# Performance work log

Measured on AMD Instinct MI355X. Metric: run time of the kernel, lower is better.

Reference implementation:

```python
import jax, jax.numpy as jnp
import numpy as np

TAU = 0.07      # temperature from __init__ default
TOP_K = 10      # hardcoded k in torch.topk
DIAG_FILL = -10.0
TOP_SIM_VAL = 0.75


def setup_inputs() -> dict:
    key = jax.random.key(0)
    k1, k2 = jax.random.split(key)
    z1 = jax.random.normal(k1, (4096, 512), dtype=jnp.float32)
    z2 = jax.random.normal(k2, (4096, 512), dtype=jnp.float32)
    return {"z1": z1, "z2": z2}


def reference(z1, z2):
    # AllGather is identity on a single device; grad_scaling=False.
    z = jnp.concatenate([z1, z2], axis=0)                      # [n, d]
    # F.normalize(dim=1): divide by L2 norm (eps-clamped)
    norm = jnp.maximum(jnp.linalg.norm(z, axis=1, keepdims=True), 1e-12)
    z = z / norm
    n = z.shape[0]
    half = n // 2

    # labels: ones at offsets +n/2 and -n/2 == identity rolled by n/2
    labels = jnp.roll(jnp.eye(n, dtype=z.dtype), half, axis=1)  # [n, n]

    sim = z @ z.T                                               # [n, n]

    # top_k_based_on_cos_sim branch: softmax of raw sim (diag still present)
    cos_sim = jax.nn.softmax(sim, axis=1)
    idx = jnp.arange(n)
    # branch mask: 0 on same-half blocks, 1 on cross-half blocks
    mask = ((idx[:, None] < half) ^ (idx[None, :] < half)).astype(z.dtype)
    cos_sim = cos_sim * mask
    _, top_idx = jax.lax.top_k(cos_sim, TOP_K)                  # [n, K]
    top_sim = jnp.zeros((n, n), dtype=z.dtype).at[idx[:, None], top_idx].set(TOP_SIM_VAL)
    labels = jnp.maximum(labels, top_sim)

    # fill diagonal with -10, scale by temperature, row log-softmax
    sim = sim.at[idx, idx].set(DIAG_FILL) / TAU
    logp = jax.nn.log_softmax(sim, axis=1)
    loss = -jnp.sum(logp * labels) / n
    return loss
```

## Files before the change

### kernel.cpp

```cpp
#include <hip/hip_runtime.h>
#include <hip/hip_bf16.h>
#include <stdint.h>

#define N_TOTAL 8192
#define HALF_N  4096
#define DIM     512
#define INV_TAU (1.0f/0.07f)

typedef __attribute__((ext_vector_type(4))) int   i32x4;

#define AS1 __attribute__((address_space(1)))
#define AS3 __attribute__((address_space(3)))

__device__ __forceinline__ uint32_t umax32(uint32_t a, uint32_t b) { return a > b ? a : b; }
__device__ __forceinline__ uint32_t umin32(uint32_t a, uint32_t b) { return a < b ? a : b; }

__device__ __forceinline__ float decode_key(uint32_t key)
{
    ushort h = (key & 0x8000u) ? (ushort)(key ^ 0x8000u) : (ushort)(key ^ 0xFFFFu);
    return (float)(*(_Float16*)&h);
}

__global__ __launch_bounds__(256) void norm_kernel(const float* __restrict__ z1,
                                                   const float* __restrict__ z2,
                                                   char* __restrict__ zq,
                                                   float* __restrict__ inv_qn,
                                                   float* __restrict__ rowsum)
{
    if (threadIdx.x < 4) rowsum[blockIdx.x * 4 + threadIdx.x] = 0.f;

    int row  = blockIdx.x * 4 + (threadIdx.x >> 6);
    int lane = threadIdx.x & 63;
    const float* src = (row < HALF_N) ? (z1 + (size_t)row * DIM)
                                      : (z2 + (size_t)(row - HALF_N) * DIM);
    const float4* p = (const float4*)src;
    float4 a = p[lane * 2];
    float4 b = p[lane * 2 + 1];
    float ss = a.x*a.x + a.y*a.y + a.z*a.z + a.w*a.w
             + b.x*b.x + b.y*b.y + b.z*b.z + b.w*b.w;
#pragma unroll
    for (int o = 1; o < 64; o <<= 1) ss += __shfl_xor(ss, o);
    float sc = 127.0f / fmaxf(sqrtf(ss), 1e-12f);

    float v[8] = {a.x*sc, a.y*sc, a.z*sc, a.w*sc, b.x*sc, b.y*sc, b.z*sc, b.w*sc};
    char c8[8];
    int qq = 0;
#pragma unroll
    for (int j = 0; j < 8; j++) {
        int qi = (int)rintf(v[j]);
        qq += qi * qi;
        c8[j] = (char)qi;
    }
#pragma unroll
    for (int o = 1; o < 64; o <<= 1) qq += __shfl_xor(qq, o);
    if (lane == 0) inv_qn[row] = 1.0f / sqrtf(fmaxf((float)qq, 1.0f));

    *(uint2*)(zq + (size_t)row * DIM + lane * 8) = *(const uint2*)c8;
}

__global__ __launch_bounds__(256, 4) void gemm_kernel(const char* __restrict__ zq,
                                                      const float* __restrict__ inv_qn,
                                                      float* __restrict__ rowsum,
                                                      uint2* __restrict__ partial,
                                                      float* __restrict__ pos_sim)
{
    int orig = blockIdx.x;
    int bid  = (orig & 7) * 260 + (orig >> 3);

    int by = (int)(64.5f - sqrtf(4160.25f - 2.0f * (float)bid));
    int off = 64 * by - (by * (by - 1)) / 2;
    if (off > bid) { --by; off = 64 * by - (by * (by - 1)) / 2; }
    else {
        int offn = 64 * (by + 1) - ((by + 1) * by) / 2;
        if (offn <= bid) { ++by; off = offn; }
    }
    int bx = by + (bid - off);

    const int brow = by * 128;
    const int bcol = bx * 128;

    __shared__ char As[2][128 * 64];
    __shared__ char Bs[2][128 * 64];

    const int t    = threadIdx.x;
    const int w    = t >> 6;
    const int lane = t & 63;
    const int wr   = w >> 1, wc = w & 1;

    i32x4 acc[4][4] = {};

    const int c0 = t, c1 = 256 + t;
    const int r0 = c0 >> 2, r1 = c1 >> 2;
    const int q0 = (c0 & 3) ^ ((r0 >> 1) & 3);
    const int q1 = (c1 & 3) ^ ((r1 >> 1) & 3);
    const size_t gaA0 = (size_t)(brow + r0) * DIM + q0 * 16;
    const size_t gaA1 = (size_t)(brow + r1) * DIM + q1 * 16;
    const size_t gaB0 = (size_t)(bcol + r0) * DIM + q0 * 16;
    const size_t gaB1 = (size_t)(bcol + r1) * DIM + q1 * 16;
    const int l0 = (w * 64) * 16;
    const int l1 = (256 + w * 64) * 16;

#define STAGE(buf, ko) do {                                                        \
    __builtin_amdgcn_global_load_lds((const AS1 uint32_t*)(zq + gaA0 + (ko)),      \
        (AS3 uint32_t*)((char*)As[buf] + l0), 16, 0, 0);                           \
    __builtin_amdgcn_global_load_lds((const AS1 uint32_t*)(zq + gaA1 + (ko)),      \
        (AS3 uint32_t*)((char*)As[buf] + l1), 16, 0, 0);                           \
    __builtin_amdgcn_global_load_lds((const AS1 uint32_t*)(zq + gaB0 + (ko)),      \
        (AS3 uint32_t*)((char*)Bs[buf] + l0), 16, 0, 0);                           \
    __builtin_amdgcn_global_load_lds((const AS1 uint32_t*)(zq + gaB1 + (ko)),      \
        (AS3 uint32_t*)((char*)Bs[buf] + l1), 16, 0, 0);                           \
} while (0)

    STAGE(0, 0);
    __syncthreads();

    int cur = 0;
    for (int kt = 0; kt < DIM / 64; ++kt) {
        if (kt + 1 < DIM / 64) STAGE(cur ^ 1, (kt + 1) * 64);

        i32x4 av[4], bv[4];
#pragma unroll
        for (int m = 0; m < 4; m++) {
            int ro = wr * 64 + m * 16 + (lane & 15);
            int s  = (lane >> 4) ^ ((ro >> 1) & 3);
            av[m] = *(const i32x4*)(As[cur] + ro * 64 + s * 16);
        }
#pragma unroll
        for (int n = 0; n < 4; n++) {
            int ro = wc * 64 + n * 16 + (lane & 15);
            int s  = (lane >> 4) ^ ((ro >> 1) & 3);
            bv[n] = *(const i32x4*)(Bs[cur] + ro * 64 + s * 16);
        }
#pragma unroll
        for (int m = 0; m < 4; m++)
#pragma unroll
            for (int n = 0; n < 4; n++)
                acc[m][n] = __builtin_amdgcn_mfma_i32_16x16x64_i8(av[m], bv[n], acc[m][n], 0, 0, 0);

        __syncthreads();
        cur ^= 1;
    }
#undef STAGE

    const bool is_cross = (brow < HALF_N) && (bcol >= HALF_N);
    const bool off_diag = (bx != by);

    float invc[4];
#pragma unroll
    for (int n = 0; n < 4; n++)
        invc[n] = inv_qn[bcol + wc * 64 + n * 16 + (lane & 15)];

    float    cs[4] = {0.f, 0.f, 0.f, 0.f};
    uint32_t s1[4] = {0u, 0u, 0u, 0u};
    uint32_t s2[4] = {0u, 0u, 0u, 0u};

#pragma unroll
    for (int m = 0; m < 4; m++) {
#pragma unroll
        for (int r = 0; r < 4; r++) {
            int grow = brow + wr * 64 + m * 16 + ((lane >> 4) << 2) + r;
            float invr = inv_qn[grow];
            float rs = 0.f;
            uint32_t t1 = 0u, t2 = 0u;
#pragma unroll
            for (int n = 0; n < 4; n++) {
                int gcol = bcol + wc * 64 + n * 16 + (lane & 15);
                float v  = (float)acc[m][n][r] * (invr * invc[n]);
                float e  = (grow == gcol) ? 0.f : __expf(v * INV_TAU);
                rs += e;
                cs[n] += e;
                if (is_cross) {
                    int cidx = gcol - HALF_N;
                    ushort h;
                    *(_Float16*)&h = (_Float16)v;
                    uint32_t key = ((uint32_t)(ushort)(h ^ (ushort)((ushort)((short)h >> 15) | 0x8000))) << 16;
                    uint32_t xr = key | (uint32_t)(4095 - cidx);
                    uint32_t mn = umin32(t1, xr);
                    t1 = umax32(t1, xr);
                    t2 = umax32(t2, mn);
                    uint32_t xc = key | (uint32_t)(4095 - grow);
                    mn = umin32(s1[n], xc);
                    s1[n] = umax32(s1[n], xc);
                    s2[n] = umax32(s2[n], mn);
                    if (cidx == grow) { pos_sim[grow] = v; pos_sim[gcol] = v; }
                }
            }
            rs += __shfl_xor(rs, 1);
            rs += __shfl_xor(rs, 2);
            rs += __shfl_xor(rs, 4);
            rs += __shfl_xor(rs, 8);
            if ((lane & 15) == 0) atomicAdd(&rowsum[grow], rs);

            if (is_cross) {
#pragma unroll
                for (int o = 1; o < 16; o <<= 1) {
                    uint32_t o1 = __shfl_xor(t1, o);
                    uint32_t o2 = __shfl_xor(t2, o);
                    uint32_t nt2 = umax32(umin32(t1, o1), umax32(t2, o2));
                    t1 = umax32(t1, o1);
                    t2 = nt2;
                }
                if ((lane & 15) == 0)
                    partial[((size_t)grow << 6) + (bx - 32) * 2 + wc] = make_uint2(t1, t2);
            }
        }
    }

    if (off_diag) {
#pragma unroll
        for (int n = 0; n < 4; n++) {
            float c = cs[n];
            c += __shfl_xor(c, 16);
            c += __shfl_xor(c, 32);
            uint32_t a1 = s1[n], a2 = s2[n];
            if (is_cross) {
#pragma unroll
                for (int o = 16; o < 64; o <<= 1) {
                    uint32_t o1 = __shfl_xor(a1, o);
                    uint32_t o2 = __shfl_xor(a2, o);
                    uint32_t nt2 = umax32(umin32(a1, o1), umax32(a2, o2));
                    a1 = umax32(a1, o1);
                    a2 = nt2;
                }
            }
            if (lane < 16) {
                int gcol = bcol + wc * 64 + n * 16 + lane;
                atomicAdd(&rowsum[gcol], c);
                if (is_cross)
                    partial[((size_t)gcol << 6) + by * 2 + wr] = make_uint2(a1, a2);
            }
        }
    }
}

__global__ __launch_bounds__(256) void topk_loss_kernel(const uint2* __restrict__ partial,
                                                        const float* __restrict__ pos_sim,
                                                        const float* __restrict__ rowsum,
                                                        float* __restrict__ contrib)
{
    int i    = blockIdx.x * 4 + (threadIdx.x >> 6);
    int lane = threadIdx.x & 63;

    uint2 p = partial[((size_t)i << 6) + lane];
    uint32_t t1 = p.x, t2 = p.y;

    int posidx = i & (HALF_N - 1);
    float S10 = 0.f; int posflag = 0;
#pragma unroll
    for (int tc = 0; tc < 10; tc++) {
        uint32_t b = umax32(t1, t2);
#pragma unroll
        for (int o = 32; o; o >>= 1)
            b = umax32(b, __shfl_xor(b, o));
        bool w1 = (b == t1);
        bool w2 = (b == t2);
        t1 = w1 ? t2 : t1;
        t2 = (w1 | w2) ? 0u : t2;

        int idx = 4095 - (int)(b & 0xFFFFu);
        S10 += decode_key(b >> 16);
        posflag |= (idx == posidx) ? 1 : 0;
    }

    if (lane == 0) {
        float ps  = pos_sim[i];
        float lse = logf(rowsum[i]);
        float L   = 1.0f + 0.75f * (10 - posflag);
        float sll = INV_TAU * (ps + 0.75f * (S10 - posflag * ps));
        contrib[i] = L * lse - sll;
    }
}

__global__ __launch_bounds__(256) void reduce_kernel(const float* __restrict__ contrib,
                                                     float* __restrict__ out)
{
    int t = threadIdx.x;
    float s = 0.f;
    for (int j = t; j < N_TOTAL; j += 256) s += contrib[j];
#pragma unroll
    for (int o = 1; o < 64; o <<= 1) s += __shfl_xor(s, o);
    __shared__ float wsum[4];
    if ((t & 63) == 0) wsum[t >> 6] = s;
    __syncthreads();
    if (t == 0) out[0] = (wsum[0] + wsum[1] + wsum[2] + wsum[3]) * (1.0f / N_TOTAL);
}

extern "C" void kernel_launch(void* const* d_in, const int* in_sizes, int n_in,
                              void* d_out, int out_size, void* d_ws, size_t ws_size,
                              hipStream_t stream)
{
    const float* z1 = (const float*)d_in[0];
    const float* z2 = (const float*)d_in[1];
    float* out = (float*)d_out;

    char* ws = (char*)d_ws;
    char*   zq      = ws;
    float*  rowsum  = (float*)(ws + 4194304);
    float*  pos_sim = (float*)(ws + 4227072);
    float*  inv_qn  = (float*)(ws + 4259840);
    uint2*  partial = (uint2*)(ws + 4292608);
    float*  contrib = (float*)(ws + 8486912);

    norm_kernel<<<N_TOTAL / 4, 256, 0, stream>>>(z1, z2, zq, inv_qn, rowsum);
    gemm_kernel<<<2080, 256, 0, stream>>>(zq, inv_qn, rowsum, partial, pos_sim);
    topk_loss_kernel<<<N_TOTAL / 4, 256, 0, stream>>>(partial, pos_sim, rowsum, contrib);
    reduce_kernel<<<1, 256, 0, stream>>>(contrib, out);
}
```

Measured before the change: 92.04 us.

## Fold temperature into exp2 scale, raise GEMM occupancy, fuse reduce into top-k kernel

The norm kernel now stores the per-row inverse norm premultiplied by log2(e)/tau, so the GEMM epilogue can call exp2 directly and skip a multiply. The raw similarity is recovered by a constant multiply only on cross blocks. Launch bounds go from 4 to 5 waves, and the column accumulators are split into two sets to shorten dependency chains. The separate reduce kernel is removed: each top-k block handles 32 rows and atomically adds its share into the output, which the norm kernel zeroes. The changes add register pressure at higher occupancy and make the final sum order nondeterministic.

```diff
diff --git a/kernel.cpp b/kernel.cpp
--- a/kernel.cpp
+++ b/kernel.cpp
@@ -6,6 +6,8 @@
 #define HALF_N  4096
 #define DIM     512
 #define INV_TAU (1.0f/0.07f)
+#define EXP2_SCALE  4.5398160046388386f
+#define SIM_FROM_VE 0.0485203026391962f
 
 typedef __attribute__((ext_vector_type(4))) int   i32x4;
 
@@ -24,10 +26,12 @@
 __global__ __launch_bounds__(256) void norm_kernel(const float* __restrict__ z1,
                                                    const float* __restrict__ z2,
                                                    char* __restrict__ zq,
-                                                   float* __restrict__ inv_qn,
-                                                   float* __restrict__ rowsum)
+                                                   float* __restrict__ inv_e,
+                                                   float* __restrict__ rowsum,
+                                                   float* __restrict__ out)
 {
     if (threadIdx.x < 4) rowsum[blockIdx.x * 4 + threadIdx.x] = 0.f;
+    if (blockIdx.x == 0 && threadIdx.x == 0) out[0] = 0.f;
 
     int row  = blockIdx.x * 4 + (threadIdx.x >> 6);
     int lane = threadIdx.x & 63;
@@ -53,13 +57,13 @@
     }
 #pragma unroll
     for (int o = 1; o < 64; o <<= 1) qq += __shfl_xor(qq, o);
-    if (lane == 0) inv_qn[row] = 1.0f / sqrtf(fmaxf((float)qq, 1.0f));
+    if (lane == 0) inv_e[row] = EXP2_SCALE / sqrtf(fmaxf((float)qq, 1.0f));
 
     *(uint2*)(zq + (size_t)row * DIM + lane * 8) = *(const uint2*)c8;
 }
 
-__global__ __launch_bounds__(256, 4) void gemm_kernel(const char* __restrict__ zq,
-                                                      const float* __restrict__ inv_qn,
+__global__ __launch_bounds__(256, 5) void gemm_kernel(const char* __restrict__ zq,
+                                                      const float* __restrict__ inv_e,
                                                       float* __restrict__ rowsum,
                                                       uint2* __restrict__ partial,
                                                       float* __restrict__ pos_sim)
@@ -148,28 +152,29 @@
     float invc[4];
 #pragma unroll
     for (int n = 0; n < 4; n++)
-        invc[n] = inv_qn[bcol + wc * 64 + n * 16 + (lane & 15)];
-
-    float    cs[4] = {0.f, 0.f, 0.f, 0.f};
-    uint32_t s1[4] = {0u, 0u, 0u, 0u};
-    uint32_t s2[4] = {0u, 0u, 0u, 0u};
+        invc[n] = inv_e[bcol + wc * 64 + n * 16 + (lane & 15)];
+
+    float    cs0[4] = {0,0,0,0}, cs1[4] = {0,0,0,0};
+    uint32_t s1a[4] = {0,0,0,0}, s2a[4] = {0,0,0,0};
+    uint32_t s1b[4] = {0,0,0,0}, s2b[4] = {0,0,0,0};
 
 #pragma unroll
     for (int m = 0; m < 4; m++) {
 #pragma unroll
         for (int r = 0; r < 4; r++) {
             int grow = brow + wr * 64 + m * 16 + ((lane >> 4) << 2) + r;
-            float invr = inv_qn[grow];
+            float invr = inv_e[grow];
             float rs = 0.f;
             uint32_t t1 = 0u, t2 = 0u;
 #pragma unroll
             for (int n = 0; n < 4; n++) {
                 int gcol = bcol + wc * 64 + n * 16 + (lane & 15);
-                float v  = (float)acc[m][n][r] * (invr * invc[n]);
-                float e  = (grow == gcol) ? 0.f : __expf(v * INV_TAU);
+                float ve = (float)acc[m][n][r] * (invr * invc[n]);
+                float e  = (grow == gcol) ? 0.f : __builtin_exp2f(ve);
                 rs += e;
-                cs[n] += e;
+                if (m < 2) cs0[n] += e; else cs1[n] += e;
                 if (is_cross) {
+                    float v = ve * SIM_FROM_VE;
                     int cidx = gcol - HALF_N;
                     ushort h;
                     *(_Float16*)&h = (_Float16)v;
@@ -179,9 +184,11 @@
                     t1 = umax32(t1, xr);
                     t2 = umax32(t2, mn);
                     uint32_t xc = key | (uint32_t)(4095 - grow);
-                    mn = umin32(s1[n], xc);
-                    s1[n] = umax32(s1[n], xc);
-                    s2[n] = umax32(s2[n], mn);
+                    if (m < 2) {
+                        mn = umin32(s1a[n], xc); s1a[n] = umax32(s1a[n], xc); s2a[n] = umax32(s2a[n], mn);
+                    } else {
+                        mn = umin32(s1b[n], xc); s1b[n] = umax32(s1b[n], xc); s2b[n] = umax32(s2b[n], mn);
+                    }
                     if (cidx == grow) { pos_sim[grow] = v; pos_sim[gcol] = v; }
                 }
             }
@@ -209,10 +216,11 @@
     if (off_diag) {
 #pragma unroll
         for (int n = 0; n < 4; n++) {
-            float c = cs[n];
+            float c = cs0[n] + cs1[n];
             c += __shfl_xor(c, 16);
             c += __shfl_xor(c, 32);
-            uint32_t a1 = s1[n], a2 = s2[n];
+            uint32_t a1 = umax32(s1a[n], s1b[n]);
+            uint32_t a2 = umax32(umin32(s1a[n], s1b[n]), umax32(s2a[n], s2b[n]));
             if (is_cross) {
 #pragma unroll
                 for (int o = 16; o < 64; o <<= 1) {
@@ -236,53 +244,50 @@
 __global__ __launch_bounds__(256) void topk_loss_kernel(const uint2* __restrict__ partial,
                                                         const float* __restrict__ pos_sim,
                                                         const float* __restrict__ rowsum,
-                                                        float* __restrict__ contrib)
-{
-    int i    = blockIdx.x * 4 + (threadIdx.x >> 6);
+                                                        float* __restrict__ out)
+{
+    int wv   = threadIdx.x >> 6;
     int lane = threadIdx.x & 63;
-
-    uint2 p = partial[((size_t)i << 6) + lane];
-    uint32_t t1 = p.x, t2 = p.y;
-
-    int posidx = i & (HALF_N - 1);
-    float S10 = 0.f; int posflag = 0;
-#pragma unroll
-    for (int tc = 0; tc < 10; tc++) {
-        uint32_t b = umax32(t1, t2);
-#pragma unroll
-        for (int o = 32; o; o >>= 1)
-            b = umax32(b, __shfl_xor(b, o));
-        bool w1 = (b == t1);
-        bool w2 = (b == t2);
-        t1 = w1 ? t2 : t1;
-        t2 = (w1 | w2) ? 0u : t2;
-
-        int idx = 4095 - (int)(b & 0xFFFFu);
-        S10 += decode_key(b >> 16);
-        posflag |= (idx == posidx) ? 1 : 0;
-    }
-
-    if (lane == 0) {
-        float ps  = pos_sim[i];
-        float lse = logf(rowsum[i]);
-        float L   = 1.0f + 0.75f * (10 - posflag);
-        float sll = INV_TAU * (ps + 0.75f * (S10 - posflag * ps));
-        contrib[i] = L * lse - sll;
-    }
-}
-
-__global__ __launch_bounds__(256) void reduce_kernel(const float* __restrict__ contrib,
-                                                     float* __restrict__ out)
-{
-    int t = threadIdx.x;
-    float s = 0.f;
-    for (int j = t; j < N_TOTAL; j += 256) s += contrib[j];
-#pragma unroll
-    for (int o = 1; o < 64; o <<= 1) s += __shfl_xor(s, o);
-    __shared__ float wsum[4];
-    if ((t & 63) == 0) wsum[t >> 6] = s;
+    float lsum = 0.f;
+
+    for (int rr = 0; rr < 8; rr++) {
+        int i = blockIdx.x * 32 + wv * 8 + rr;
+
+        uint2 p = partial[((size_t)i << 6) + lane];
+        uint32_t t1 = p.x, t2 = p.y;
+
+        int posidx = i & (HALF_N - 1);
+        float S10 = 0.f; int posflag = 0;
+#pragma unroll
+        for (int tc = 0; tc < 10; tc++) {
+            uint32_t b = umax32(t1, t2);
+#pragma unroll
+            for (int o = 32; o; o >>= 1)
+                b = umax32(b, __shfl_xor(b, o));
+            bool w1 = (b == t1);
+            bool w2 = (b == t2);
+            t1 = w1 ? t2 : t1;
+            t2 = (w1 | w2) ? 0u : t2;
+
+            int idx = 4095 - (int)(b & 0xFFFFu);
+            S10 += decode_key(b >> 16);
+            posflag |= (idx == posidx) ? 1 : 0;
+        }
+
+        if (lane == 0) {
+            float ps  = pos_sim[i];
+            float lse = logf(rowsum[i]);
+            float L   = 1.0f + 0.75f * (10 - posflag);
+            float sll = INV_TAU * (ps + 0.75f * (S10 - posflag * ps));
+            lsum += L * lse - sll;
+        }
+    }
+
+    __shared__ float bsum[4];
+    if (lane == 0) bsum[wv] = lsum;
     __syncthreads();
-    if (t == 0) out[0] = (wsum[0] + wsum[1] + wsum[2] + wsum[3]) * (1.0f / N_TOTAL);
+    if (threadIdx.x == 0)
+        atomicAdd(out, (bsum[0] + bsum[1] + bsum[2] + bsum[3]) * (1.0f / N_TOTAL));
 }
 
 extern "C" void kernel_launch(void* const* d_in, const int* in_sizes, int n_in,
@@ -297,12 +302,10 @@
     char*   zq      = ws;
     float*  rowsum  = (float*)(ws + 4194304);
     float*  pos_sim = (float*)(ws + 4227072);
-    float*  inv_qn  = (float*)(ws + 4259840);
+    float*  inv_e   = (float*)(ws + 4259840);
     uint2*  partial = (uint2*)(ws + 4292608);
-    float*  contrib = (float*)(ws + 8486912);
-
-    norm_kernel<<<N_TOTAL / 4, 256, 0, stream>>>(z1, z2, zq, inv_qn, rowsum);
-    gemm_kernel<<<2080, 256, 0, stream>>>(zq, inv_qn, rowsum, partial, pos_sim);
-    topk_loss_kernel<<<N_TOTAL / 4, 256, 0, stream>>>(partial, pos_sim, rowsum, contrib);
-    reduce_kernel<<<1, 256, 0, stream>>>(contrib, out);
-}
+
+    norm_kernel<<<N_TOTAL / 4, 256, 0, stream>>>(z1, z2, zq, inv_e, rowsum, out);
+    gemm_kernel<<<2080, 256, 0, stream>>>(zq, inv_e, rowsum, partial, pos_sim);
+    topk_loss_kernel<<<N_TOTAL / 32, 256, 0, stream>>>(partial, pos_sim, rowsum, out);
+}
```

After: 138.6 us. +50.6%, slower.
